# Kernel optimization log

Hardware: AMD Instinct MI355X
Metric: run time of the kernel (lower is better)

## Reference

```python
import jax, jax.numpy as jnp
import numpy as np

B, L, D = 64, 1024, 1024


def _attn(q, K, V, mask):
    # q: [B,D], K/V: [B,L,D], mask: [B,L] bool (True = valid)
    scores = jnp.einsum('bd,bld->bl', q, K) / jnp.sqrt(jnp.asarray(D, q.dtype))
    scores = jnp.where(mask, scores, -jnp.inf)
    attn = jax.nn.softmax(scores, axis=-1)
    attn = jnp.where(jnp.isnan(attn), 0.0, attn)  # torch.nan_to_num for all-masked rows
    return jnp.einsum('bl,bld->bd', attn, V)


def setup_inputs() -> dict:
    key = jax.random.key(0)
    ks = jax.random.split(key, 12)
    xav = float(np.sqrt(6.0 / (D + D)))  # xavier_uniform for square Linear
    img_mask = jax.random.randint(ks[4], (B, L), 0, 2).astype(bool)
    txt_mask = jax.random.randint(ks[7], (B, L), 0, 2).astype(bool)
    # guarantee at least one valid token per row
    img_mask = img_mask.at[:, 0].set(True)
    txt_mask = txt_mask.at[:, 0].set(True)
    return {
        'img_q': jax.random.normal(ks[0], (B, D), jnp.float32),
        'txt_q': jax.random.normal(ks[1], (B, D), jnp.float32),
        'K_img': jax.random.normal(ks[2], (B, L, D), jnp.float32),
        'V_img': jax.random.normal(ks[3], (B, L, D), jnp.float32),
        'img_mask': img_mask,
        'K_txt': jax.random.normal(ks[5], (B, L, D), jnp.float32),
        'V_txt': jax.random.normal(ks[6], (B, L, D), jnp.float32),
        'txt_mask': txt_mask,
        'W_img': jax.random.uniform(ks[8], (D, D), jnp.float32, -xav, xav),
        'b_img': jnp.zeros((D,), jnp.float32),
        'W_txt': jax.random.uniform(ks[9], (D, D), jnp.float32, -xav, xav),
        'b_txt': jnp.zeros((D,), jnp.float32),
    }


def reference(img_q, txt_q, K_img, V_img, img_mask, K_txt, V_txt, txt_mask,
              W_img, b_img, W_txt, b_txt):
    # Dropout is identity in eval mode.
    ctx_img = _attn(txt_q, K_img, V_img, img_mask)
    img_q = img_q + ctx_img @ W_img.T + b_img
    ctx_txt = _attn(img_q, K_txt, V_txt, txt_mask)
    txt_q = txt_q + ctx_txt @ W_txt.T + b_txt
    return (img_q, txt_q)
```

## Files before the change

### kernel.cpp

```cpp
#include <hip/hip_runtime.h>
#include <hip/hip_bf16.h>
#include <float.h>

#define B_ 64
#define L_ 1024
#define D_ 1024
#define NSPLIT 16
#define CHUNK 64
#define PSTRIDE 1028

typedef __bf16 bf16x8 __attribute__((ext_vector_type(8)));
typedef float f32x4 __attribute__((ext_vector_type(4)));

__device__ inline unsigned short f2bf(float x) {
    unsigned int u = __float_as_uint(x);
    unsigned int lsb = (u >> 16) & 1u;
    u += 0x7fffu + lsb;
    return (unsigned short)(u >> 16);
}

__global__ __launch_bounds__(256) void attn_partial_kernel(
    const float* __restrict__ q,
    const float* __restrict__ K,
    const float* __restrict__ V,
    const int*   __restrict__ mask,
    float* __restrict__ part)
{
    const int bid  = blockIdx.x;
    const int b    = bid >> 4;
    const int sp   = bid & 15;
    const int l0   = sp * CHUNK;
    const int tid  = threadIdx.x;
    const int wave = tid >> 6;
    const int lane = tid & 63;

    __shared__ float qs[D_];
    __shared__ float sc[CHUNK];
    __shared__ float pv[CHUNK];

    float4 qv = reinterpret_cast<const float4*>(q + (size_t)b * D_)[tid];
    reinterpret_cast<float4*>(qs)[tid] = qv;
    __syncthreads();

    const float4* qrow = reinterpret_cast<const float4*>(qs);
    for (int r = 0; r < 16; ++r) {
        int l  = wave * 16 + r;
        int gl = l0 + l;
        int mv = mask[(size_t)b * L_ + gl];
        if (!mv) { if (lane == 0) sc[l] = -FLT_MAX; continue; }
        const float4* krow = reinterpret_cast<const float4*>(K + ((size_t)b * L_ + gl) * D_);
        float acc = 0.f;
        #pragma unroll
        for (int rep = 0; rep < 4; ++rep) {
            float4 kv = krow[lane + rep * 64];
            float4 qq = qrow[lane + rep * 64];
            acc += kv.x * qq.x + kv.y * qq.y + kv.z * qq.z + kv.w * qq.w;
        }
        #pragma unroll
        for (int off = 32; off > 0; off >>= 1) acc += __shfl_xor(acc, off, 64);
        if (lane == 0) sc[l] = acc * 0.03125f;
    }
    __syncthreads();

    float m = -FLT_MAX;
    #pragma unroll
    for (int l = 0; l < CHUNK; ++l) m = fmaxf(m, sc[l]);

    if (tid < CHUNK) {
        float s = sc[tid];
        pv[tid] = (s == -FLT_MAX) ? 0.f : __expf(s - m);
    }
    __syncthreads();

    float se = 0.f;
    float ax = 0.f, ay = 0.f, az = 0.f, aw = 0.f;
    const float4* vbase = reinterpret_cast<const float4*>(V + ((size_t)b * L_ + l0) * D_);
    for (int l = 0; l < CHUNK; ++l) {
        float pl = pv[l];
        se += pl;
        if (pl == 0.f) continue;
        float4 vv = vbase[l * (D_ / 4) + tid];
        ax += pl * vv.x; ay += pl * vv.y; az += pl * vv.z; aw += pl * vv.w;
    }

    float* po = part + (size_t)bid * PSTRIDE;
    float4 o; o.x = ax; o.y = ay; o.z = az; o.w = aw;
    reinterpret_cast<float4*>(po)[tid] = o;
    if (tid == 0) { po[D_] = m; po[D_ + 1] = se; }
}

__global__ __launch_bounds__(256) void combine_kernel(
    const float* __restrict__ part,
    unsigned short* __restrict__ ctxb)
{
    const int b   = blockIdx.x;
    const int tid = threadIdx.x;
    const float* pb = part + (size_t)b * NSPLIT * PSTRIDE;

    float ms[NSPLIT];
    float gm = -FLT_MAX;
    #pragma unroll
    for (int sp = 0; sp < NSPLIT; ++sp) {
        ms[sp] = pb[(size_t)sp * PSTRIDE + D_];
        gm = fmaxf(gm, ms[sp]);
    }
    float sca[NSPLIT];
    float denom = 0.f;
    #pragma unroll
    for (int sp = 0; sp < NSPLIT; ++sp) {
        float e = (ms[sp] == -FLT_MAX) ? 0.f : __expf(ms[sp] - gm);
        sca[sp] = e;
        denom += pb[(size_t)sp * PSTRIDE + D_ + 1] * e;
    }
    float inv = 1.f / denom;

    float ax = 0.f, ay = 0.f, az = 0.f, aw = 0.f;
    #pragma unroll
    for (int sp = 0; sp < NSPLIT; ++sp) {
        if (sca[sp] == 0.f) continue;
        float4 o = reinterpret_cast<const float4*>(pb + (size_t)sp * PSTRIDE)[tid];
        float s = sca[sp] * inv;
        ax += s * o.x; ay += s * o.y; az += s * o.z; aw += s * o.w;
    }
    ushort4 u;
    u.x = f2bf(ax); u.y = f2bf(ay); u.z = f2bf(az); u.w = f2bf(aw);
    reinterpret_cast<ushort4*>(ctxb)[(size_t)b * (D_ / 4) + tid] = u;
}

__global__ __launch_bounds__(256) void convert_kernel(
    const float* __restrict__ src, unsigned short* __restrict__ dst, int n4)
{
    int i = blockIdx.x * 256 + threadIdx.x;
    if (i >= n4) return;
    float4 v = reinterpret_cast<const float4*>(src)[i];
    ushort4 u;
    u.x = f2bf(v.x); u.y = f2bf(v.y); u.z = f2bf(v.z); u.w = f2bf(v.w);
    reinterpret_cast<ushort4*>(dst)[i] = u;
}

__global__ __launch_bounds__(256) void proj_kernel(
    const unsigned short* __restrict__ Abf,
    const unsigned short* __restrict__ Wbf,
    const float* __restrict__ qin,
    const float* __restrict__ bias,
    float* __restrict__ out)
{
    const int tid  = threadIdx.x;
    const int wave = tid >> 6;
    const int lane = tid & 63;
    const int m0   = (blockIdx.x & 3) * 16;
    const int n0   = (blockIdx.x >> 2) * 16;
    const int r    = lane & 15;
    const int g    = lane >> 4;

    const bf16x8* aptr = reinterpret_cast<const bf16x8*>(
        Abf + (size_t)(m0 + r) * D_ + g * 8 + wave * 256);
    const bf16x8* bptr = reinterpret_cast<const bf16x8*>(
        Wbf + (size_t)(n0 + r) * D_ + g * 8 + wave * 256);

    f32x4 acc = {0.f, 0.f, 0.f, 0.f};
    #pragma unroll
    for (int kk = 0; kk < 8; ++kk) {
        bf16x8 a  = aptr[kk * 4];
        bf16x8 bb = bptr[kk * 4];
        acc = __builtin_amdgcn_mfma_f32_16x16x32_bf16(a, bb, acc, 0, 0, 0);
    }

    __shared__ float red[1024];
    #pragma unroll
    for (int i = 0; i < 4; ++i) red[wave * 256 + lane * 4 + i] = acc[i];
    __syncthreads();

    int ol = tid >> 2, oi = tid & 3;
    float v = red[ol * 4 + oi] + red[256 + ol * 4 + oi]
            + red[512 + ol * 4 + oi] + red[768 + ol * 4 + oi];
    int row = m0 + ((ol >> 4) * 4 + oi);
    int col = n0 + (ol & 15);
    out[(size_t)row * D_ + col] = qin[(size_t)row * D_ + col] + bias[col] + v;
}

extern "C" void kernel_launch(void* const* d_in, const int* in_sizes, int n_in,
                              void* d_out, int out_size, void* d_ws, size_t ws_size,
                              hipStream_t stream) {
    const float* img_q    = (const float*)d_in[0];
    const float* txt_q    = (const float*)d_in[1];
    const float* K_img    = (const float*)d_in[2];
    const float* V_img    = (const float*)d_in[3];
    const int*   img_mask = (const int*)  d_in[4];
    const float* K_txt    = (const float*)d_in[5];
    const float* V_txt    = (const float*)d_in[6];
    const int*   txt_mask = (const int*)  d_in[7];
    const float* W_img    = (const float*)d_in[8];
    const float* b_img    = (const float*)d_in[9];
    const float* W_txt    = (const float*)d_in[10];
    const float* b_txt    = (const float*)d_in[11];

    float* out_img = (float*)d_out;
    float* out_txt = (float*)d_out + B_ * D_;

    char* ws = (char*)d_ws;
    float* part = (float*)ws;
    size_t part_bytes = (size_t)B_ * NSPLIT * PSTRIDE * sizeof(float);
    unsigned short* Wimg_bf = (unsigned short*)(ws + part_bytes);
    unsigned short* Wtxt_bf = Wimg_bf + (size_t)D_ * D_;
    unsigned short* ctx_bf  = Wtxt_bf + (size_t)D_ * D_;

    convert_kernel<<<1024, 256, 0, stream>>>(W_img, Wimg_bf, D_ * D_ / 4);
    convert_kernel<<<1024, 256, 0, stream>>>(W_txt, Wtxt_bf, D_ * D_ / 4);

    attn_partial_kernel<<<B_ * NSPLIT, 256, 0, stream>>>(txt_q, K_img, V_img, img_mask, part);
    combine_kernel<<<B_, 256, 0, stream>>>(part, ctx_bf);
    proj_kernel<<<256, 256, 0, stream>>>(ctx_bf, Wimg_bf, img_q, b_img, out_img);

    attn_partial_kernel<<<B_ * NSPLIT, 256, 0, stream>>>(out_img, K_txt, V_txt, txt_mask, part);
    combine_kernel<<<B_, 256, 0, stream>>>(part, ctx_bf);
    proj_kernel<<<256, 256, 0, stream>>>(ctx_bf, Wtxt_bf, txt_q, b_txt, out_txt);
}
```

Measured before the change: 151.1 us.

## Compact valid mask indices and batch K/V loads for memory-level parallelism

Each block ballots the mask and builds a compacted list of valid row indices, so K dot products and V accumulation visit only valid rows. The list is padded to a multiple of 8 with a valid index whose weight is zero. K rows are processed two per wave, and V rows eight at a time with all loads issued before the FMAs, to keep more memory requests in flight. q is held in registers instead of LDS, and launch bounds request 4 blocks per CU. The extra registers for the batched loads could limit occupancy.

```diff
diff --git a/kernel.cpp b/kernel.cpp
--- a/kernel.cpp
+++ b/kernel.cpp
@@ -19,7 +19,7 @@
     return (unsigned short)(u >> 16);
 }
 
-__global__ __launch_bounds__(256) void attn_partial_kernel(
+__global__ __launch_bounds__(256, 4) void attn_partial_kernel(
     const float* __restrict__ q,
     const float* __restrict__ K,
     const float* __restrict__ V,
@@ -34,53 +34,78 @@
     const int wave = tid >> 6;
     const int lane = tid & 63;
 
-    __shared__ float qs[D_];
+    __shared__ int   vidx[CHUNK];
     __shared__ float sc[CHUNK];
-    __shared__ float pv[CHUNK];
-
-    float4 qv = reinterpret_cast<const float4*>(q + (size_t)b * D_)[tid];
-    reinterpret_cast<float4*>(qs)[tid] = qv;
-    __syncthreads();
-
-    const float4* qrow = reinterpret_cast<const float4*>(qs);
-    for (int r = 0; r < 16; ++r) {
-        int l  = wave * 16 + r;
-        int gl = l0 + l;
-        int mv = mask[(size_t)b * L_ + gl];
-        if (!mv) { if (lane == 0) sc[l] = -FLT_MAX; continue; }
-        const float4* krow = reinterpret_cast<const float4*>(K + ((size_t)b * L_ + gl) * D_);
-        float acc = 0.f;
+    __shared__ float pw[CHUNK];
+    __shared__ int   nvalid;
+
+    const float4* qptr = reinterpret_cast<const float4*>(q + (size_t)b * D_);
+    float4 qreg[4];
+    #pragma unroll
+    for (int rep = 0; rep < 4; ++rep) qreg[rep] = qptr[lane + rep * 64];
+
+    if (wave == 0) {
+        int mv = mask[(size_t)b * L_ + l0 + lane];
+        unsigned long long bal = __ballot(mv != 0);
+        int nv   = __popcll(bal);
+        int padv = bal ? (__ffsll((long long)bal) - 1) : 0;
+        int rank = __popcll(bal & ((1ull << lane) - 1));
+        if (mv) vidx[rank] = lane;
+        if (lane >= nv) vidx[lane] = padv;
+        if (lane == 0) nvalid = nv;
+    }
+    __syncthreads();
+    const int nv  = nvalid;
+    const int nvp = (nv + 7) & ~7;
+
+    const float* Kb = K + ((size_t)b * L_ + l0) * D_;
+    for (int jj = wave; jj < nvp; jj += 8) {
+        int j2 = jj + 4;
+        const float4* k0 = reinterpret_cast<const float4*>(Kb + (size_t)vidx[jj] * D_);
+        const float4* k1 = reinterpret_cast<const float4*>(Kb + (size_t)vidx[j2] * D_);
+        float a0 = 0.f, a1 = 0.f;
+        float4 kv0[4], kv1[4];
+        #pragma unroll
+        for (int rep = 0; rep < 4; ++rep) { kv0[rep] = k0[lane + rep * 64];
+                                            kv1[rep] = k1[lane + rep * 64]; }
         #pragma unroll
         for (int rep = 0; rep < 4; ++rep) {
-            float4 kv = krow[lane + rep * 64];
-            float4 qq = qrow[lane + rep * 64];
-            acc += kv.x * qq.x + kv.y * qq.y + kv.z * qq.z + kv.w * qq.w;
+            a0 += kv0[rep].x * qreg[rep].x + kv0[rep].y * qreg[rep].y
+                + kv0[rep].z * qreg[rep].z + kv0[rep].w * qreg[rep].w;
+            a1 += kv1[rep].x * qreg[rep].x + kv1[rep].y * qreg[rep].y
+                + kv1[rep].z * qreg[rep].z + kv1[rep].w * qreg[rep].w;
         }
         #pragma unroll
-        for (int off = 32; off > 0; off >>= 1) acc += __shfl_xor(acc, off, 64);
-        if (lane == 0) sc[l] = acc * 0.03125f;
+        for (int off = 32; off > 0; off >>= 1) {
+            a0 += __shfl_xor(a0, off, 64);
+            a1 += __shfl_xor(a1, off, 64);
+        }
+        if (lane == 0) { sc[jj] = a0 * 0.03125f; sc[j2] = a1 * 0.03125f; }
     }
     __syncthreads();
 
     float m = -FLT_MAX;
-    #pragma unroll
-    for (int l = 0; l < CHUNK; ++l) m = fmaxf(m, sc[l]);
-
-    if (tid < CHUNK) {
-        float s = sc[tid];
-        pv[tid] = (s == -FLT_MAX) ? 0.f : __expf(s - m);
-    }
+    for (int j = 0; j < nv; ++j) m = fmaxf(m, sc[j]);
+
+    if (tid < CHUNK) pw[tid] = (tid < nv) ? __expf(sc[tid] - m) : 0.f;
     __syncthreads();
 
     float se = 0.f;
     float ax = 0.f, ay = 0.f, az = 0.f, aw = 0.f;
     const float4* vbase = reinterpret_cast<const float4*>(V + ((size_t)b * L_ + l0) * D_);
-    for (int l = 0; l < CHUNK; ++l) {
-        float pl = pv[l];
-        se += pl;
-        if (pl == 0.f) continue;
-        float4 vv = vbase[l * (D_ / 4) + tid];
-        ax += pl * vv.x; ay += pl * vv.y; az += pl * vv.z; aw += pl * vv.w;
+    for (int j = 0; j < nvp; j += 8) {
+        float p[8]; int ix[8];
+        #pragma unroll
+        for (int t = 0; t < 8; ++t) { p[t] = pw[j + t]; ix[t] = vidx[j + t]; }
+        float4 vv[8];
+        #pragma unroll
+        for (int t = 0; t < 8; ++t) vv[t] = vbase[(size_t)ix[t] * (D_ / 4) + tid];
+        #pragma unroll
+        for (int t = 0; t < 8; ++t) {
+            se += p[t];
+            ax += p[t] * vv[t].x; ay += p[t] * vv[t].y;
+            az += p[t] * vv[t].z; aw += p[t] * vv[t].w;
+        }
     }
 
     float* po = part + (size_t)bid * PSTRIDE;
```

New measurement: 139.9 us. 7.4% less time.
